# Kernel tuning notes

Measured on AMD Instinct MI355X. Metric: run time of the kernel, lower is better.

The kernel has to match this reference:

```python
import jax, jax.numpy as jnp
import numpy as np
from jax import lax

# ReplicationPad1d (left,right) per kernel size, matching Python round((ks-1)/2)
PADS = {2: (0, 1), 3: (1, 1), 6: (2, 3), 12: (6, 5)}

B, N, T, C, OC, E = 8, 1024, 64, 16, 16, 16384


def setup_inputs() -> dict:
    key = jax.random.key(0)
    ks = jax.random.split(key, 16)

    def wn(k, shape, fan_in):
        return jax.random.normal(k, shape, jnp.float32) / jnp.sqrt(jnp.float32(fan_in))

    inp = {
        "x": jax.random.normal(ks[0], (B, N, T, C), jnp.float32),
        "edge_index": jax.random.randint(ks[1], (2, E), 0, N, dtype=jnp.int32),
        # temporal conv branches (Conv1d: [out_ch, in_ch, ks])
        "w_t2": wn(ks[2], (OC, C, 2), C * 2), "b_t2": jnp.zeros((OC,), jnp.float32),
        "w_t3": wn(ks[3], (OC, C, 3), C * 3), "b_t3": jnp.zeros((OC,), jnp.float32),
        "w_t6": wn(ks[4], (OC, C, 6), C * 6), "b_t6": jnp.zeros((OC,), jnp.float32),
        "w_t12": wn(ks[5], (OC, C, 12), C * 12), "b_t12": jnp.zeros((OC,), jnp.float32),
        # GCNConv: lin weight [out, in] (no bias in lin), separate bias
        "w_gcn": wn(ks[6], (OC, C), C), "b_gcn": jnp.zeros((OC,), jnp.float32),
        # slin: Linear(T -> T)
        "w_slin": wn(ks[7], (T, T), T), "b_slin": jnp.zeros((T,), jnp.float32),
    }
    return inp


def reference(x, edge_index, w_t2, b_t2, w_t3, b_t3, w_t6, b_t6, w_t12, b_t12,
              w_gcn, b_gcn, w_slin, b_slin):
    Bd, Nd, Td, Cd = x.shape
    # ---- temporal multi-scale Conv1d branches ----
    xt = x.reshape(Bd * Nd, Td, Cd).transpose(0, 2, 1)  # [BN, C, T]
    outs = []
    for w, b in ((w_t2, b_t2), (w_t3, b_t3), (w_t6, b_t6), (w_t12, b_t12)):
        kern = w.shape[-1]
        l, r = PADS[kern]
        xp = jnp.pad(xt, ((0, 0), (0, 0), (l, r)), mode="edge")  # replication pad
        y = lax.conv_general_dilated(xp, w, (1,), "VALID",
                                     dimension_numbers=("NCH", "OIH", "NCH"))
        outs.append((y + b[None, :, None]).transpose(0, 2, 1))  # [BN, T, OC]
    out_t = jnp.concatenate(outs, axis=-1).reshape(Bd, Nd, Td, -1)  # [B,N,T,4*OC]

    # ---- GCNConv spatial branch (gather-transform-scatter) ----
    xs = x.transpose(0, 2, 1, 3)                         # [B,T,N,C]
    xl = jnp.einsum("btnc,oc->btno", xs, w_gcn)          # [B,T,N,OC]
    row, col = edge_index[0], edge_index[1]
    deg = jnp.zeros((Nd,), x.dtype).at[col].add(1.0) + 1.0  # +1 self loop
    dinv = lax.rsqrt(deg)
    norm = dinv[row] * dinv[col]                         # [E]
    msgs = xl[:, :, row, :] * norm[None, None, :, None]  # gather [B,T,E,OC]
    agg = jnp.zeros_like(xl).at[:, :, col, :].add(msgs)  # scatter-add
    agg = agg + (dinv * dinv)[None, None, :, None] * xl + b_gcn  # self loops + bias

    xs_out = agg.transpose(0, 2, 3, 1)                   # [B,N,OC,T]
    xs_out = jnp.einsum("bnot,st->bnos", xs_out, w_slin) + b_slin
    xs_out = xs_out.transpose(0, 1, 3, 2)                # [B,N,T,OC]

    return jnp.tanh(jnp.concatenate([out_t, xs_out], axis=-1))  # [B,N,T,embed_dim]
```

## Files before the change

kernel.cpp:

```cpp
#include <hip/hip_runtime.h>
#include <hip/hip_bf16.h>

#define BB  8
#define NN  1024
#define TT  64
#define CC  16
#define OCC 16
#define EE  16384
#define CHO 80

typedef float  f32x4  __attribute__((ext_vector_type(4)));
typedef __bf16 bf16x8 __attribute__((ext_vector_type(8)));

static __device__ __forceinline__ float tanh_fast(float v) {
    float e = __expf(2.0f * v);
    return 1.0f - 2.0f * __builtin_amdgcn_rcpf(e + 1.0f);
}
static __device__ __forceinline__ unsigned pk_bf16(float a, float b) {
    unsigned short lo = __builtin_bit_cast(unsigned short, (__bf16)a);
    unsigned short hi = __builtin_bit_cast(unsigned short, (__bf16)b);
    return (unsigned)lo | ((unsigned)hi << 16);
}
static __device__ __forceinline__ float bflo(unsigned u) { return __uint_as_float(u << 16); }
static __device__ __forceinline__ float bfhi(unsigned u) { return __uint_as_float(u & 0xFFFF0000u); }

static __device__ __forceinline__ void acc8(float* ac, int base, float w, float4 v) {
    unsigned ux = __float_as_uint(v.x), uy = __float_as_uint(v.y);
    unsigned uz = __float_as_uint(v.z), uw = __float_as_uint(v.w);
    ac[base + 0] = fmaf(w, bflo(ux), ac[base + 0]);
    ac[base + 1] = fmaf(w, bfhi(ux), ac[base + 1]);
    ac[base + 2] = fmaf(w, bflo(uy), ac[base + 2]);
    ac[base + 3] = fmaf(w, bfhi(uy), ac[base + 3]);
    ac[base + 4] = fmaf(w, bflo(uz), ac[base + 4]);
    ac[base + 5] = fmaf(w, bfhi(uz), ac[base + 5]);
    ac[base + 6] = fmaf(w, bflo(uw), ac[base + 6]);
    ac[base + 7] = fmaf(w, bfhi(uw), ac[base + 7]);
}


__global__ __launch_bounds__(1024) void k_prep(
    const int* __restrict__ ei, const float* __restrict__ x,
    const float* __restrict__ w2,  const float* __restrict__ b2,
    const float* __restrict__ w3,  const float* __restrict__ b3,
    const float* __restrict__ w6,  const float* __restrict__ b6,
    const float* __restrict__ w12, const float* __restrict__ b12,
    const float* __restrict__ wg,  const float* __restrict__ bg,
    const float* __restrict__ wsl,
    int* __restrict__ offg, int* __restrict__ cntg, float* __restrict__ dinvg,
    int* __restrict__ src, float* __restrict__ wE,
    float* __restrict__ wgT, float* __restrict__ bgp, float* __restrict__ bcat,
    __bf16* __restrict__ wslh, __bf16* __restrict__ wsll, __bf16* __restrict__ wtg,
    __bf16* __restrict__ xb) {
    int tid = threadIdx.x, bid = blockIdx.x;
    const float* wsrc[4] = {w2, w3, w6, w12};
    const float* bsrc[4] = {b2, b3, b6, b12};
    const int ksA[4] = {2, 3, 6, 12};
    const int plA[4] = {0, 1, 2, 6};
    if (bid >= 14) {
        int e4 = (bid - 14) * 1024 + tid;
        float4 u = ((const float4*)x)[e4];
        uint2 w;
        w.x = pk_bf16(u.x, u.y);
        w.y = pk_bf16(u.z, u.w);
        ((uint2*)xb)[e4] = w;
        return;
    }
    if (bid == 13) {
        if (tid < 256) wgT[tid] = wg[(tid & 15) * CC + (tid >> 4)];
        else if (tid < 272) bgp[tid - 256] = bg[tid - 256];
        else if (tid < 336) { int j = tid - 272; bcat[j] = bsrc[j >> 4][j & 15]; }
        for (int e = tid; e < 4096; e += 1024) {
            float v = wsl[e];
            __bf16 h = (__bf16)v;
            wslh[e] = h;
            wsll[e] = (__bf16)(v - (float)h);
        }
        return;
    }
    if (bid != 0) {
        int e = (bid - 1) * 1024 + tid;
        int j = e / 192, kk = e - j * 192;
        int d = kk >> 4, c = kk & 15;
        int br = j >> 4, oc = j & 15;
        int k = d - 6 + plA[br];
        float v = (k >= 0 && k < ksA[br]) ? wsrc[br][oc * (CC * ksA[br]) + c * ksA[br] + k] : 0.0f;
        wtg[e] = (__bf16)v;
        return;
    }
    __shared__ int   h[NN];
    __shared__ int   sc[NN];
    __shared__ int   cur[NN];
    __shared__ float dl[NN];
    h[tid] = 0;
    __syncthreads();
    for (int e = tid; e < EE; e += 1024) atomicAdd(&h[ei[EE + e]], 1);
    __syncthreads();
    int v = h[tid];
    sc[tid] = v;
    __syncthreads();
    for (int d = 1; d < NN; d <<= 1) {
        int add = (tid >= d) ? sc[tid - d] : 0;
        __syncthreads();
        sc[tid] += add;
        __syncthreads();
    }
    int oex = sc[tid] - v;
    float dv = rsqrtf((float)v + 1.0f);
    offg[tid] = oex; cntg[tid] = v; dinvg[tid] = dv;
    cur[tid] = oex; dl[tid] = dv;
    __syncthreads();
    for (int e = tid; e < EE; e += 1024) {
        int r = ei[e], c = ei[EE + e];
        int i = atomicAdd(&cur[c], 1);
        src[i] = r;
        wE[i]  = dl[r] * dl[c];
    }
}


__global__ __launch_bounds__(256) void k_tconv(
    const __bf16* __restrict__ xb, const __bf16* __restrict__ wtg,
    const float* __restrict__ bcat, float* __restrict__ out) {
    __shared__ __align__(16) __bf16 xs[4][76 * 24];
    int tid = threadIdx.x;
    int wave = tid >> 6, lane = tid & 63;
    int l15 = lane & 15, g = lane >> 4;
    int bq = blockIdx.x & 7, nq = blockIdx.x >> 3;

    bf16x8 afr[6];
#pragma unroll
    for (int s = 0; s < 6; s++) {
        const __bf16* p = wtg + (wave * 16 + l15) * 192 + s * 32 + g * 8;
        afr[s] = __builtin_bit_cast(bf16x8, *(const float4*)p);
    }
    float4 bias = *(const float4*)(bcat + wave * 16 + g * 4);

    {
        int t = tid >> 2, c0 = (tid & 3) * 4;
#pragma unroll
        for (int node = 0; node < 4; node++) {
            size_t bn = (size_t)bq * NN + nq * 4 + node;
            uint2 w = *(const uint2*)(xb + bn * (TT * CC) + tid * 4);
            *(uint2*)(xs[node] + (t + 6) * 24 + c0) = w;
            if (t == 0) {
#pragma unroll
                for (int r = 0; r < 6; r++) *(uint2*)(xs[node] + r * 24 + c0) = w;
            }
            if (t == 63) {
#pragma unroll
                for (int r = 70; r < 76; r++) *(uint2*)(xs[node] + r * 24 + c0) = w;
            }
        }
    }
    __syncthreads();

    for (int node = 0; node < 4; node++) {
        size_t bn = (size_t)bq * NN + nq * 4 + node;
        f32x4 acc[4];
#pragma unroll
        for (int m = 0; m < 4; m++) acc[m] = (f32x4){bias.x, bias.y, bias.z, bias.w};
#pragma unroll
        for (int m = 0; m < 4; m++) {
#pragma unroll
            for (int s = 0; s < 6; s++) {
                const __bf16* p = xs[node] + (m * 16 + l15 + 2 * s + (g >> 1)) * 24 + (g & 1) * 8;
                bf16x8 b = __builtin_bit_cast(bf16x8, *(const float4*)p);
                acc[m] = __builtin_amdgcn_mfma_f32_16x16x32_bf16(afr[s], b, acc[m], 0, 0, 0);
            }
        }
#pragma unroll
        for (int m = 0; m < 4; m++) {
            float4 o;
            o.x = tanh_fast(acc[m][0]); o.y = tanh_fast(acc[m][1]);
            o.z = tanh_fast(acc[m][2]); o.w = tanh_fast(acc[m][3]);
            *(float4*)(out + (bn * TT + m * 16 + l15) * CHO + wave * 16 + g * 4) = o;
        }
    }
}


__global__ __launch_bounds__(256) void k_gcn(
    const __bf16* __restrict__ xb,
    const int* __restrict__ off, const int* __restrict__ cnt,
    const int* __restrict__ src, const float* __restrict__ wE, const float* __restrict__ dinv,
    const float* __restrict__ wgT, const float* __restrict__ bgp,
    const __bf16* __restrict__ wslh, const __bf16* __restrict__ wsll,
    const float* __restrict__ bsl, float* __restrict__ out) {
    __shared__ __align__(16) __bf16 xh[4][16 * 72];
    __shared__ __align__(16) __bf16 xl2[4][16 * 72];
    int tid = threadIdx.x;
    int wave = tid >> 6, lane = tid & 63;
    int l15 = lane & 15, g = lane >> 4;
    int b = blockIdx.x & 7, nq = blockIdx.x >> 3;
    int n = nq * 4 + wave;

    int sglob = wave * 16 + l15;
    bf16x8 bh[2], bl[2];
#pragma unroll
    for (int k = 0; k < 2; k++) {
        bh[k] = __builtin_bit_cast(bf16x8, *(const float4*)(wslh + sglob * 64 + k * 32 + g * 8));
        bl[k] = __builtin_bit_cast(bf16x8, *(const float4*)(wsll + sglob * 64 + k * 32 + g * 8));
    }

    float ac[16];
    const __bf16* xbb = xb + (size_t)b * NN * (TT * CC);
    {
        int o0 = off[n], cn_ = cnt[n];
        float d = dinv[n], d2 = d * d;
        const __bf16* st = xbb + (size_t)n * (TT * CC) + lane * 16;
        float4 s0 = *(const float4*)st;
        float4 s1 = *(const float4*)(st + 8);
        {
            unsigned ux = __float_as_uint(s0.x), uy = __float_as_uint(s0.y);
            unsigned uz = __float_as_uint(s0.z), uw = __float_as_uint(s0.w);
            ac[0] = d2 * bflo(ux); ac[1] = d2 * bfhi(ux);
            ac[2] = d2 * bflo(uy); ac[3] = d2 * bfhi(uy);
            ac[4] = d2 * bflo(uz); ac[5] = d2 * bfhi(uz);
            ac[6] = d2 * bflo(uw); ac[7] = d2 * bfhi(uw);
            ux = __float_as_uint(s1.x); uy = __float_as_uint(s1.y);
            uz = __float_as_uint(s1.z); uw = __float_as_uint(s1.w);
            ac[8]  = d2 * bflo(ux); ac[9]  = d2 * bfhi(ux);
            ac[10] = d2 * bflo(uy); ac[11] = d2 * bfhi(uy);
            ac[12] = d2 * bflo(uz); ac[13] = d2 * bfhi(uz);
            ac[14] = d2 * bflo(uw); ac[15] = d2 * bfhi(uw);
        }
        const int* srcp = src + o0;
        const float* wEp = wE + o0;
        int j = 0;
        for (; j + 2 <= cn_; j += 2) {
            int sA = srcp[j], sB = srcp[j + 1];
            float wA = wEp[j], wB = wEp[j + 1];
            const __bf16* pa = xbb + (size_t)sA * (TT * CC) + lane * 16;
            const __bf16* pb = xbb + (size_t)sB * (TT * CC) + lane * 16;
            float4 a0 = *(const float4*)pa, a1 = *(const float4*)(pa + 8);
            float4 b0 = *(const float4*)pb, b1 = *(const float4*)(pb + 8);
            acc8(ac, 0, wA, a0); acc8(ac, 8, wA, a1);
            acc8(ac, 0, wB, b0); acc8(ac, 8, wB, b1);
        }
        if (j < cn_) {
            int sA = srcp[j];
            float wA = wEp[j];
            const __bf16* pa = xbb + (size_t)sA * (TT * CC) + lane * 16;
            float4 a0 = *(const float4*)pa, a1 = *(const float4*)(pa + 8);
            acc8(ac, 0, wA, a0); acc8(ac, 8, wA, a1);
        }
    }

#pragma unroll
    for (int o = 0; o < 16; o++) {
        float pv = bgp[o];
#pragma unroll
        for (int c = 0; c < 16; c++) pv = fmaf(wgT[c * 16 + o], ac[c], pv);
        __bf16 h = (__bf16)pv;
        xh[wave][o * 72 + lane]  = h;
        xl2[wave][o * 72 + lane] = (__bf16)(pv - (float)h);
    }
    __syncthreads();

    float bv = bsl[sglob];
    for (int node = 0; node < 4; node++) {
        f32x4 acc = (f32x4){bv, bv, bv, bv};
        bf16x8 ah[2], al[2];
#pragma unroll
        for (int k = 0; k < 2; k++) {
            ah[k] = __builtin_bit_cast(bf16x8, *(const float4*)(xh[node]  + l15 * 72 + k * 32 + g * 8));
            al[k] = __builtin_bit_cast(bf16x8, *(const float4*)(xl2[node] + l15 * 72 + k * 32 + g * 8));
        }
#pragma unroll
        for (int k = 0; k < 2; k++) {
            acc = __builtin_amdgcn_mfma_f32_16x16x32_bf16(ah[k], bh[k], acc, 0, 0, 0);
            acc = __builtin_amdgcn_mfma_f32_16x16x32_bf16(al[k], bh[k], acc, 0, 0, 0);
            acc = __builtin_amdgcn_mfma_f32_16x16x32_bf16(ah[k], bl[k], acc, 0, 0, 0);
        }
        float4 o4;
        o4.x = tanh_fast(acc[0]); o4.y = tanh_fast(acc[1]);
        o4.z = tanh_fast(acc[2]); o4.w = tanh_fast(acc[3]);
        size_t bn = (size_t)b * NN + nq * 4 + node;
        *(float4*)(out + (bn * TT + sglob) * CHO + 64 + g * 4) = o4;
    }
}


extern "C" void kernel_launch(void* const* d_in, const int* in_sizes, int n_in,
                              void* d_out, int out_size, void* d_ws, size_t ws_size,
                              hipStream_t stream) {
    const float* x   = (const float*)d_in[0];
    const int*   ei  = (const int*)d_in[1];
    const float* w2  = (const float*)d_in[2];
    const float* b2  = (const float*)d_in[3];
    const float* w3  = (const float*)d_in[4];
    const float* b3  = (const float*)d_in[5];
    const float* w6  = (const float*)d_in[6];
    const float* b6  = (const float*)d_in[7];
    const float* w12 = (const float*)d_in[8];
    const float* b12 = (const float*)d_in[9];
    const float* wg  = (const float*)d_in[10];
    const float* bg  = (const float*)d_in[11];
    const float* wsl = (const float*)d_in[12];
    const float* bsl = (const float*)d_in[13];
    float* out = (float*)d_out;

    char*   ws   = (char*)d_ws;
    int*    off  = (int*)(ws);
    int*    cnt  = (int*)(ws + 4096);
    float*  dinv = (float*)(ws + 8192);
    int*    src  = (int*)(ws + 12288);
    float*  wE   = (float*)(ws + 77824);
    float*  wgT  = (float*)(ws + 143360);
    float*  bgp  = (float*)(ws + 144384);
    float*  bcat = (float*)(ws + 144448);
    __bf16* wslh = (__bf16*)(ws + 144704);
    __bf16* wsll = (__bf16*)(ws + 152896);
    __bf16* wtg  = (__bf16*)(ws + 161088);
    __bf16* xb   = (__bf16*)(ws + 4194304);

    k_prep<<<2062, 1024, 0, stream>>>(ei, x, w2, b2, w3, b3, w6, b6, w12, b12, wg, bg, wsl,
                                      off, cnt, dinv, src, wE, wgT, bgp, bcat,
                                      wslh, wsll, wtg, xb);
    k_tconv<<<BB * NN / 4, 256, 0, stream>>>(xb, wtg, bcat, out);
    k_gcn<<<BB * NN / 4, 256, 0, stream>>>(xb, off, cnt, src, wE, dinv, wgT, bgp,
                                           wslh, wsll, bsl, out);
}
```

Measured before the change: 100.4 us.

## Fuse temporal conv and GCN kernels into one launch sharing LDS

Merges k_tconv and k_gcn into a single k_main kernel. Both used the same block/node mapping, so one launch now does both, with a single shared-memory buffer reused between the two phases. This removes a kernel launch and the tail/drain gap between the kernels, and the block's x tile may still be cache-warm for the GCN phase. It also widens the edge-gather unroll from 2 to 4 for more memory-level parallelism, at the cost of more registers and possibly lower occupancy.

New measurement: 94.87 us (median of 3 runs). 5.5% less time.

```diff
diff --git a/kernel.cpp b/kernel.cpp
--- a/kernel.cpp
+++ b/kernel.cpp
@@ -118,14 +118,21 @@
 }
 
 
-__global__ __launch_bounds__(256) void k_tconv(
+__global__ __launch_bounds__(256) void k_main(
     const __bf16* __restrict__ xb, const __bf16* __restrict__ wtg,
-    const float* __restrict__ bcat, float* __restrict__ out) {
-    __shared__ __align__(16) __bf16 xs[4][76 * 24];
+    const float* __restrict__ bcat,
+    const int* __restrict__ off, const int* __restrict__ cnt,
+    const int* __restrict__ src, const float* __restrict__ wE, const float* __restrict__ dinv,
+    const float* __restrict__ wgT, const float* __restrict__ bgp,
+    const __bf16* __restrict__ wslh, const __bf16* __restrict__ wsll,
+    const float* __restrict__ bsl, float* __restrict__ out) {
+    __shared__ __align__(16) char smem[18432];
     int tid = threadIdx.x;
     int wave = tid >> 6, lane = tid & 63;
     int l15 = lane & 15, g = lane >> 4;
     int bq = blockIdx.x & 7, nq = blockIdx.x >> 3;
+    int n = nq * 4 + wave;
+    const __bf16* xbb = xb + (size_t)bq * NN * (TT * CC);
 
     bf16x8 afr[6];
 #pragma unroll
@@ -139,22 +146,23 @@
         int t = tid >> 2, c0 = (tid & 3) * 4;
 #pragma unroll
         for (int node = 0; node < 4; node++) {
-            size_t bn = (size_t)bq * NN + nq * 4 + node;
-            uint2 w = *(const uint2*)(xb + bn * (TT * CC) + tid * 4);
-            *(uint2*)(xs[node] + (t + 6) * 24 + c0) = w;
+            __bf16* xsn = (__bf16*)(smem + node * 3648);
+            uint2 w = *(const uint2*)(xbb + (size_t)(nq * 4 + node) * (TT * CC) + tid * 4);
+            *(uint2*)(xsn + (t + 6) * 24 + c0) = w;
             if (t == 0) {
 #pragma unroll
-                for (int r = 0; r < 6; r++) *(uint2*)(xs[node] + r * 24 + c0) = w;
+                for (int r = 0; r < 6; r++) *(uint2*)(xsn + r * 24 + c0) = w;
             }
             if (t == 63) {
 #pragma unroll
-                for (int r = 70; r < 76; r++) *(uint2*)(xs[node] + r * 24 + c0) = w;
+                for (int r = 70; r < 76; r++) *(uint2*)(xsn + r * 24 + c0) = w;
             }
         }
     }
     __syncthreads();
 
     for (int node = 0; node < 4; node++) {
+        const __bf16* xsn = (const __bf16*)(smem + node * 3648);
         size_t bn = (size_t)bq * NN + nq * 4 + node;
         f32x4 acc[4];
 #pragma unroll
@@ -163,7 +171,7 @@
         for (int m = 0; m < 4; m++) {
 #pragma unroll
             for (int s = 0; s < 6; s++) {
-                const __bf16* p = xs[node] + (m * 16 + l15 + 2 * s + (g >> 1)) * 24 + (g & 1) * 8;
+                const __bf16* p = xsn + (m * 16 + l15 + 2 * s + (g >> 1)) * 24 + (g & 1) * 8;
                 bf16x8 b = __builtin_bit_cast(bf16x8, *(const float4*)p);
                 acc[m] = __builtin_amdgcn_mfma_f32_16x16x32_bf16(afr[s], b, acc[m], 0, 0, 0);
             }
@@ -176,34 +184,8 @@
             *(float4*)(out + (bn * TT + m * 16 + l15) * CHO + wave * 16 + g * 4) = o;
         }
     }
-}
-
-
-__global__ __launch_bounds__(256) void k_gcn(
-    const __bf16* __restrict__ xb,
-    const int* __restrict__ off, const int* __restrict__ cnt,
-    const int* __restrict__ src, const float* __restrict__ wE, const float* __restrict__ dinv,
-    const float* __restrict__ wgT, const float* __restrict__ bgp,
-    const __bf16* __restrict__ wslh, const __bf16* __restrict__ wsll,
-    const float* __restrict__ bsl, float* __restrict__ out) {
-    __shared__ __align__(16) __bf16 xh[4][16 * 72];
-    __shared__ __align__(16) __bf16 xl2[4][16 * 72];
-    int tid = threadIdx.x;
-    int wave = tid >> 6, lane = tid & 63;
-    int l15 = lane & 15, g = lane >> 4;
-    int b = blockIdx.x & 7, nq = blockIdx.x >> 3;
-    int n = nq * 4 + wave;
-
-    int sglob = wave * 16 + l15;
-    bf16x8 bh[2], bl[2];
-#pragma unroll
-    for (int k = 0; k < 2; k++) {
-        bh[k] = __builtin_bit_cast(bf16x8, *(const float4*)(wslh + sglob * 64 + k * 32 + g * 8));
-        bl[k] = __builtin_bit_cast(bf16x8, *(const float4*)(wsll + sglob * 64 + k * 32 + g * 8));
-    }
 
     float ac[16];
-    const __bf16* xbb = xb + (size_t)b * NN * (TT * CC);
     {
         int o0 = off[n], cn_ = cnt[n];
         float d = dinv[n], d2 = d * d;
@@ -227,17 +209,23 @@
         const int* srcp = src + o0;
         const float* wEp = wE + o0;
         int j = 0;
-        for (; j + 2 <= cn_; j += 2) {
-            int sA = srcp[j], sB = srcp[j + 1];
-            float wA = wEp[j], wB = wEp[j + 1];
+        for (; j + 4 <= cn_; j += 4) {
+            int sA = srcp[j], sB = srcp[j + 1], sC = srcp[j + 2], sD = srcp[j + 3];
+            float wA = wEp[j], wB = wEp[j + 1], wC = wEp[j + 2], wD = wEp[j + 3];
             const __bf16* pa = xbb + (size_t)sA * (TT * CC) + lane * 16;
             const __bf16* pb = xbb + (size_t)sB * (TT * CC) + lane * 16;
+            const __bf16* pc = xbb + (size_t)sC * (TT * CC) + lane * 16;
+            const __bf16* pd = xbb + (size_t)sD * (TT * CC) + lane * 16;
             float4 a0 = *(const float4*)pa, a1 = *(const float4*)(pa + 8);
             float4 b0 = *(const float4*)pb, b1 = *(const float4*)(pb + 8);
+            float4 c0 = *(const float4*)pc, c1 = *(const float4*)(pc + 8);
+            float4 d0 = *(const float4*)pd, d1 = *(const float4*)(pd + 8);
             acc8(ac, 0, wA, a0); acc8(ac, 8, wA, a1);
             acc8(ac, 0, wB, b0); acc8(ac, 8, wB, b1);
-        }
-        if (j < cn_) {
+            acc8(ac, 0, wC, c0); acc8(ac, 8, wC, c1);
+            acc8(ac, 0, wD, d0); acc8(ac, 8, wD, d1);
+        }
+        for (; j < cn_; j++) {
             int sA = srcp[j];
             float wA = wEp[j];
             const __bf16* pa = xbb + (size_t)sA * (TT * CC) + lane * 16;
@@ -246,25 +234,45 @@
         }
     }
 
+    float pv[16];
 #pragma unroll
     for (int o = 0; o < 16; o++) {
-        float pv = bgp[o];
-#pragma unroll
-        for (int c = 0; c < 16; c++) pv = fmaf(wgT[c * 16 + o], ac[c], pv);
-        __bf16 h = (__bf16)pv;
-        xh[wave][o * 72 + lane]  = h;
-        xl2[wave][o * 72 + lane] = (__bf16)(pv - (float)h);
-    }
-    __syncthreads();
-
+        float p = bgp[o];
+#pragma unroll
+        for (int c = 0; c < 16; c++) p = fmaf(wgT[c * 16 + o], ac[c], p);
+        pv[o] = p;
+    }
+    __syncthreads();
+
+    {
+        __bf16* xhn = (__bf16*)(smem + wave * 4608);
+        __bf16* xln = (__bf16*)(smem + wave * 4608 + 2304);
+#pragma unroll
+        for (int o = 0; o < 16; o++) {
+            __bf16 h = (__bf16)pv[o];
+            xhn[o * 72 + lane] = h;
+            xln[o * 72 + lane] = (__bf16)(pv[o] - (float)h);
+        }
+    }
+    __syncthreads();
+
+    int sglob = wave * 16 + l15;
+    bf16x8 bh[2], bl[2];
+#pragma unroll
+    for (int k = 0; k < 2; k++) {
+        bh[k] = __builtin_bit_cast(bf16x8, *(const float4*)(wslh + sglob * 64 + k * 32 + g * 8));
+        bl[k] = __builtin_bit_cast(bf16x8, *(const float4*)(wsll + sglob * 64 + k * 32 + g * 8));
+    }
     float bv = bsl[sglob];
     for (int node = 0; node < 4; node++) {
+        const __bf16* xhn = (const __bf16*)(smem + node * 4608);
+        const __bf16* xln = (const __bf16*)(smem + node * 4608 + 2304);
         f32x4 acc = (f32x4){bv, bv, bv, bv};
         bf16x8 ah[2], al[2];
 #pragma unroll
         for (int k = 0; k < 2; k++) {
-            ah[k] = __builtin_bit_cast(bf16x8, *(const float4*)(xh[node]  + l15 * 72 + k * 32 + g * 8));
-            al[k] = __builtin_bit_cast(bf16x8, *(const float4*)(xl2[node] + l15 * 72 + k * 32 + g * 8));
+            ah[k] = __builtin_bit_cast(bf16x8, *(const float4*)(xhn + l15 * 72 + k * 32 + g * 8));
+            al[k] = __builtin_bit_cast(bf16x8, *(const float4*)(xln + l15 * 72 + k * 32 + g * 8));
         }
 #pragma unroll
         for (int k = 0; k < 2; k++) {
@@ -275,7 +283,7 @@
         float4 o4;
         o4.x = tanh_fast(acc[0]); o4.y = tanh_fast(acc[1]);
         o4.z = tanh_fast(acc[2]); o4.w = tanh_fast(acc[3]);
-        size_t bn = (size_t)b * NN + nq * 4 + node;
+        size_t bn = (size_t)bq * NN + nq * 4 + node;
         *(float4*)(out + (bn * TT + sglob) * CHO + 64 + g * 4) = o4;
     }
 }
@@ -317,7 +325,6 @@
     k_prep<<<2062, 1024, 0, stream>>>(ei, x, w2, b2, w3, b3, w6, b6, w12, b12, wg, bg, wsl,
                                       off, cnt, dinv, src, wE, wgT, bgp, bcat,
                                       wslh, wsll, wtg, xb);
-    k_tconv<<<BB * NN / 4, 256, 0, stream>>>(xb, wtg, bcat, out);
-    k_gcn<<<BB * NN / 4, 256, 0, stream>>>(xb, off, cnt, src, wE, dinv, wgT, bgp,
-                                           wslh, wsll, bsl, out);
-}
+    k_main<<<BB * NN / 4, 256, 0, stream>>>(xb, wtg, bcat, off, cnt, src, wE, dinv,
+                                            wgT, bgp, wslh, wsll, bsl, out);
+}
```
